# Optimization experiments

Hardware: AMD Instinct MI355X
Metric: run time of the kernel (lower is better)

## Reference

```python
import jax, jax.numpy as jnp
import numpy as np

N, E, B, H, L = 100000, 200000, 2048, 256, 4
EPS_MSG = 1e-7   # GENConv message eps
LN_EPS = 1e-5    # torch LayerNorm default eps
SM_EPS = 1e-16   # PyG softmax denominator eps


def layer_norm(x, g, b):
    mu = x.mean(-1, keepdims=True)
    var = ((x - mu) ** 2).mean(-1, keepdims=True)
    return (x - mu) * jax.lax.rsqrt(var + LN_EPS) * g + b


def gen_conv(x, src, dst, eattr, t, W1, b1, lg, lb, W2, b2):
    # GENConv(aggr='softmax', learn_t, num_layers=2, norm='layer')
    msg = jax.nn.relu(x[src] + eattr) + EPS_MSG                      # [E,H]
    scaled = msg * t
    seg_max = jax.ops.segment_max(scaled, dst, num_segments=N)       # [N,H]
    seg_max = jnp.where(jnp.isfinite(seg_max), seg_max, 0.0)
    ex = jnp.exp(scaled - seg_max[dst])                              # [E,H]
    denom = jax.ops.segment_sum(ex, dst, num_segments=N)             # [N,H]
    alpha = ex / (denom[dst] + SM_EPS)
    out = jax.ops.segment_sum(msg * alpha, dst, num_segments=N)      # [N,H]
    out = out + x                                                    # root residual inside GENConv
    h = jax.nn.relu(layer_norm(out @ W1 + b1, lg, lb))               # MLP: Lin -> LN -> ReLU -> Lin
    return h @ W2 + b2


def setup_inputs() -> dict:
    key = jax.random.key(0)
    ks = iter(jax.random.split(key, 16))
    s = lambda *sh: jax.random.normal(next(ks), sh, jnp.float32) * 0.05
    return dict(
        x=jax.random.normal(next(ks), (N, 9), jnp.float32),
        edge_index=jax.random.randint(next(ks), (2, E), 0, N),
        edge_attr=jax.random.normal(next(ks), (E, 3), jnp.float32),
        batch=jnp.sort(jax.random.randint(next(ks), (N,), 0, B)),
        node_W=s(9, H), node_b=jnp.zeros((H,), jnp.float32),
        edge_W=s(3, H), edge_b=jnp.zeros((H,), jnp.float32),
        vn_emb=jnp.zeros((1, H), jnp.float32),
        ln_g=jnp.ones((L, H), jnp.float32), ln_b=jnp.zeros((L, H), jnp.float32),
        t=jnp.ones((L - 1,), jnp.float32),
        mlp_W1=s(L - 1, H, 2 * H), mlp_b1=jnp.zeros((L - 1, 2 * H), jnp.float32),
        mlp_ln_g=jnp.ones((L - 1, 2 * H), jnp.float32), mlp_ln_b=jnp.zeros((L - 1, 2 * H), jnp.float32),
        mlp_W2=s(L - 1, 2 * H, H), mlp_b2=jnp.zeros((L - 1, H), jnp.float32),
    )


def reference(x, edge_index, edge_attr, batch, node_W, node_b, edge_W, edge_b,
              vn_emb, ln_g, ln_b, t, mlp_W1, mlp_b1, mlp_ln_g, mlp_ln_b, mlp_W2, mlp_b2):
    src, dst = edge_index[0], edge_index[1]
    h = x @ node_W + node_b                                          # node encoder
    ea = edge_attr @ edge_W + edge_b                                 # edge encoder
    vn = jnp.broadcast_to(vn_emb, (B, H))
    counts = jax.ops.segment_sum(jnp.ones((N,), h.dtype), batch, num_segments=B)
    inv_counts = (1.0 / jnp.maximum(counts, 1.0))[:, None]           # [B,1]
    # layers[1:] run conv (block='res+'); layers[0] supplies only the final norm+act
    for l in range(1, L):
        hn = jax.nn.relu(layer_norm(h, ln_g[l], ln_b[l]))            # dropout=0.1 is a no-op in eval
        h = h + gen_conv(hn, src, dst, ea, t[l - 1],
                         mlp_W1[l - 1], mlp_b1[l - 1], mlp_ln_g[l - 1], mlp_ln_b[l - 1],
                         mlp_W2[l - 1], mlp_b2[l - 1])
        vn = vn + jax.ops.segment_sum(h, batch, num_segments=B) * inv_counts  # scatter_mean
        h = h + vn[batch]                                            # broadcast virtual node
    h = jax.nn.relu(layer_norm(h, ln_g[0], ln_b[0]))
    return jax.ops.segment_sum(h, batch, num_segments=B) * inv_counts  # global_mean_pool [B,H]
```

## Files before the change

### kernel.cpp

```cpp
#include <hip/hip_runtime.h>
#include <cstdint>
#include <cstddef>


typedef _Float16 half8_t __attribute__((ext_vector_type(8)));
typedef _Float16 half4_t __attribute__((ext_vector_type(4)));
typedef float    floatx4 __attribute__((ext_vector_type(4)));

#define DEVINL __device__ __forceinline__

DEVINL float wave_sum(float v) {
#pragma unroll
  for (int m = 32; m; m >>= 1) v += __shfl_xor(v, m, 64);
  return v;
}

__global__ __launch_bounds__(256) void k_node_enc(
    const float* __restrict__ x, const float* __restrict__ W,
    const float* __restrict__ bias, _Float16* __restrict__ h, int Nr) {
  __shared__ float sW[9 * 256];
  __shared__ float sb[256];
  __shared__ float sx[72];
  const int j = threadIdx.x;
#pragma unroll
  for (int k = 0; k < 9; ++k) sW[k * 256 + j] = W[k * 256 + j];
  sb[j] = bias[j];
  const int row0 = blockIdx.x * 8;
  if (j < 72) {
    int p = row0 * 9 + j;
    sx[j] = (p < Nr * 9) ? x[p] : 0.f;
  }
  __syncthreads();
  for (int r = 0; r < 8; ++r) {
    int row = row0 + r;
    if (row >= Nr) break;
    float acc = sb[j];
#pragma unroll
    for (int k = 0; k < 9; ++k) acc = fmaf(sx[r * 9 + k], sW[k * 256 + j], acc);
    h[(size_t)row * 256 + j] = (_Float16)acc;
  }
}

__global__ void k_bptr(const int* __restrict__ batch, int* __restrict__ bptr,
                       int N_, int B_) {
  int b = blockIdx.x * 256 + threadIdx.x;
  if (b > B_) return;
  int lo = 0, hi = N_;
  while (lo < hi) {
    int mid = (lo + hi) >> 1;
    if (batch[mid] < b) lo = mid + 1; else hi = mid;
  }
  bptr[b] = lo;
}

__global__ void k_deg(const int* __restrict__ ei, int* __restrict__ deg, int E_) {
  int e = blockIdx.x * 256 + threadIdx.x;
  if (e < E_) atomicAdd(&deg[ei[E_ + e]], 1);
}

__global__ __launch_bounds__(256) void k_scan1(
    const int* __restrict__ in, int* __restrict__ out1, int* __restrict__ bsum, int n) {
  __shared__ int tmp[256];
  const int t = threadIdx.x;
  const int base = blockIdx.x * 1024;
  int v[4];
  int run = 0;
#pragma unroll
  for (int i = 0; i < 4; ++i) {
    int p = base + t * 4 + i;
    int xv = (p < n) ? in[p] : 0;
    run += xv;
    v[i] = run;
  }
  tmp[t] = run;
  __syncthreads();
  for (int off = 1; off < 256; off <<= 1) {
    int u = (t >= off) ? tmp[t - off] : 0;
    __syncthreads();
    tmp[t] += u;
    __syncthreads();
  }
  int excl = tmp[t] - run;
#pragma unroll
  for (int i = 0; i < 4; ++i) {
    int p = base + t * 4 + i;
    if (p < n) out1[p] = v[i] + excl;
  }
  if (t == 255) bsum[blockIdx.x] = tmp[255];
}

__global__ void k_scan2(int* bsum, int nb, int* ptr0) {
  if (threadIdx.x == 0 && blockIdx.x == 0) {
    int run = 0;
    for (int i = 0; i < nb; ++i) { int xv = bsum[i]; bsum[i] = run; run += xv; }
    ptr0[0] = 0;
  }
}

__global__ __launch_bounds__(256) void k_scan3(int* out1, const int* __restrict__ bsum, int n) {
  int add = bsum[blockIdx.x];
  int p0 = blockIdx.x * 1024 + threadIdx.x * 4;
#pragma unroll
  for (int i = 0; i < 4; ++i) {
    int p = p0 + i;
    if (p < n) out1[p] += add;
  }
}

__global__ void k_copy(const int* __restrict__ a, int* __restrict__ b, int n) {
  int i = blockIdx.x * 256 + threadIdx.x;
  if (i < n) b[i] = a[i];
}

__global__ void k_csrfill(const int* __restrict__ ei, int* __restrict__ cursor,
                          int* __restrict__ csr_src, int* __restrict__ csr_eid, int E_) {
  int e = blockIdx.x * 256 + threadIdx.x;
  if (e < E_) {
    int d = ei[E_ + e];
    int pos = atomicAdd(&cursor[d], 1);
    csr_src[pos] = ei[e];
    csr_eid[pos] = e;
  }
}

__global__ void k_vninit(const float* __restrict__ emb, float* __restrict__ vn) {
  vn[(size_t)blockIdx.x * 256 + threadIdx.x] = emb[threadIdx.x];
}

__global__ __launch_bounds__(256) void k_wcvt_all(
    const float* __restrict__ W1, const float* __restrict__ W2,
    _Float16* __restrict__ W1T, _Float16* __restrict__ W2T) {
  int idx = blockIdx.x * 256 + threadIdx.x;
  int mat = idx >> 17;
  int rem = idx & 131071;
  if (mat < 3) {
    int k = rem >> 9, n = rem & 511;
    W1T[(size_t)mat * 131072 + (size_t)n * 256 + k] =
        (_Float16)W1[(size_t)mat * 131072 + rem];
  } else {
    int m = mat - 3;
    int k = rem >> 8, n = rem & 255;
    W2T[(size_t)m * 131072 + (size_t)n * 512 + k] =
        (_Float16)W2[(size_t)m * 131072 + rem];
  }
}

__global__ __launch_bounds__(256) void k_ln256(
    const _Float16* __restrict__ h, const float* __restrict__ g,
    const float* __restrict__ b, _Float16* __restrict__ out, int Nr) {
  int row = blockIdx.x * 4 + (threadIdx.x >> 6);
  if (row >= Nr) return;
  int lane = threadIdx.x & 63;
  half4_t xh = *(const half4_t*)(h + (size_t)row * 256 + lane * 4);
  float x0 = (float)xh[0], x1 = (float)xh[1], x2 = (float)xh[2], x3 = (float)xh[3];
  float s = wave_sum(x0 + x1 + x2 + x3);
  float mu = s * (1.f / 256.f);
  float d0 = x0 - mu, d1 = x1 - mu, d2 = x2 - mu, d3 = x3 - mu;
  float v = wave_sum(d0 * d0 + d1 * d1 + d2 * d2 + d3 * d3);
  float rstd = rsqrtf(v * (1.f / 256.f) + 1e-5f);
  float4 gv = *(const float4*)(g + lane * 4);
  float4 bv = *(const float4*)(b + lane * 4);
  half4_t o;
  o[0] = (_Float16)fmaxf(d0 * rstd * gv.x + bv.x, 0.f);
  o[1] = (_Float16)fmaxf(d1 * rstd * gv.y + bv.y, 0.f);
  o[2] = (_Float16)fmaxf(d2 * rstd * gv.z + bv.z, 0.f);
  o[3] = (_Float16)fmaxf(d3 * rstd * gv.w + bv.w, 0.f);
  *(half4_t*)(out + (size_t)row * 256 + lane * 4) = o;
}

__global__ __launch_bounds__(256) void k_aggregate(
    const _Float16* __restrict__ hn, const float* __restrict__ eattr,
    const float* __restrict__ edgeW, const float* __restrict__ edgeB,
    const int* __restrict__ indptr, const int* __restrict__ csr_src,
    const int* __restrict__ csr_eid, const float* __restrict__ tptr,
    _Float16* __restrict__ agg, int Nr) {
  int node = blockIdx.x * 4 + (threadIdx.x >> 6);
  if (node >= Nr) return;
  int lane = threadIdx.x & 63;
  int j0 = lane * 4;
  float4 w0 = *(const float4*)(edgeW + j0);
  float4 w1 = *(const float4*)(edgeW + 256 + j0);
  float4 w2 = *(const float4*)(edgeW + 512 + j0);
  float4 wb = *(const float4*)(edgeB + j0);
  float W0[4] = {w0.x, w0.y, w0.z, w0.w};
  float W1r[4] = {w1.x, w1.y, w1.z, w1.w};
  float W2r[4] = {w2.x, w2.y, w2.z, w2.w};
  float WB[4] = {wb.x, wb.y, wb.z, wb.w};
  float tval = tptr[0];
  int e0 = indptr[node], e1 = indptr[node + 1];
  float D[4] = {0.f, 0.f, 0.f, 0.f};
  float Nu[4] = {0.f, 0.f, 0.f, 0.f};
  for (int s = e0; s < e1; ++s) {
    int srcn = csr_src[s];
    int eid = csr_eid[s];
    float ex0 = eattr[(size_t)eid * 3 + 0];
    float ex1 = eattr[(size_t)eid * 3 + 1];
    float ex2 = eattr[(size_t)eid * 3 + 2];
    half4_t hv = *(const half4_t*)(hn + (size_t)srcn * 256 + j0);
#pragma unroll
    for (int i = 0; i < 4; ++i) {
      float eaj = fmaf(ex0, W0[i], fmaf(ex1, W1r[i], fmaf(ex2, W2r[i], WB[i])));
      float msg = fmaxf((float)hv[i] + eaj, 0.f) + 1e-7f;
      float pr = __expf(msg * tval);
      D[i] += pr;
      Nu[i] = fmaf(pr, msg, Nu[i]);
    }
  }
  half4_t hs = *(const half4_t*)(hn + (size_t)node * 256 + j0);
  half4_t res;
#pragma unroll
  for (int i = 0; i < 4; ++i)
    res[i] = (_Float16)(Nu[i] / (D[i] + 1e-16f) + (float)hs[i]);
  *(half4_t*)(agg + (size_t)node * 256 + j0) = res;
}

__global__ __launch_bounds__(256, 3) void k_gemm1(
    const _Float16* __restrict__ A, const _Float16* __restrict__ BT,
    const float* __restrict__ bias, _Float16* __restrict__ outh,
    float2* __restrict__ rstat, int M) {
  __shared__ _Float16 ldsA[64 * 256];
  __shared__ _Float16 ldsB[128 * 64];
  const int tid = threadIdx.x;
  const int lane = tid & 63;
  const int wv = tid >> 6;
  const int m0 = blockIdx.x * 64;
  const int wm = wv * 16;
  const int q = lane >> 4;
  const int l16 = lane & 15;

  {
    half8_t tmp[8];
    int ss[8];
#pragma unroll
    for (int g = 0; g < 8; ++g) {
      int s = g * 256 + tid;
      int r = s >> 5;
      int c = (s & 31) ^ (r & 7);
      int rowA = m0 + r;
      rowA = rowA < M ? rowA : (M - 1);
      tmp[g] = *(const half8_t*)(A + (size_t)rowA * 256 + c * 8);
      ss[g] = s;
    }
#pragma unroll
    for (int g = 0; g < 8; ++g)
      *(half8_t*)(ldsA + (size_t)ss[g] * 8) = tmp[g];
  }

  size_t offB[4];
  int ldsOffB[4];
#pragma unroll
  for (int i = 0; i < 4; ++i) {
    int p = (i * 4 + wv) * 64 + lane;
    int r = p >> 3;
    int s = p & 7;
    int gg = s ^ (r & 7);
    offB[i] = (size_t)r * 256 + gg * 8;
    ldsOffB[i] = p * 8;
  }
  half8_t rb[4];
  auto loadB = [&](int j) {
    int n = j >> 2, t = j & 3;
    size_t base = (size_t)n * 128 * 256 + t * 64;
#pragma unroll
    for (int i = 0; i < 4; ++i)
      rb[i] = *(const half8_t*)(BT + base + offB[i]);
  };
  auto writeB = [&]() {
#pragma unroll
    for (int i = 0; i < 4; ++i)
      *(half8_t*)(ldsB + ldsOffB[i]) = rb[i];
  };

  floatx4 acc[8] = {};
  float sA[4] = {0.f, 0.f, 0.f, 0.f}, s2A[4] = {0.f, 0.f, 0.f, 0.f};

  loadB(0);
  writeB();
  for (int j = 0; j < 16; ++j) {
    __syncthreads();
    if (j + 1 < 16) loadB(j + 1);
    const int t = j & 3;
#pragma unroll
    for (int kk = 0; kk < 2; ++kk) {
      const int c8 = kk * 4 + q;
      const int cg = t * 8 + c8;
      int r = wm + l16;
      half8_t af = *(const half8_t*)(ldsA + (size_t)(r * 32 + (cg ^ (r & 7))) * 8);
      half8_t bf[8];
#pragma unroll
      for (int ct = 0; ct < 8; ++ct) {
        int n = ct * 16 + l16;
        bf[ct] = *(const half8_t*)(ldsB + (size_t)(n * 8 + (c8 ^ (n & 7))) * 8);
      }
#pragma unroll
      for (int ct = 0; ct < 8; ++ct)
        acc[ct] = __builtin_amdgcn_mfma_f32_16x16x32_f16(af, bf[ct], acc[ct], 0, 0, 0);
    }
    __syncthreads();
    if (j + 1 < 16) writeB();
    if ((j & 3) == 3) {
      int n = j >> 2;
#pragma unroll
      for (int rr = 0; rr < 4; ++rr) {
        int row = m0 + wm + q * 4 + rr;
        float vv[8];
        float s = 0.f, s2 = 0.f;
#pragma unroll
        for (int ct = 0; ct < 8; ++ct) {
          int col = n * 128 + ct * 16 + l16;
          float v = acc[ct][rr] + bias[col];
          vv[ct] = v;
          s += v;
          s2 += v * v;
        }
        if (row < M) {
#pragma unroll
          for (int ct = 0; ct < 8; ++ct) {
            int col = n * 128 + ct * 16 + l16;
            outh[(size_t)row * 512 + col] = (_Float16)vv[ct];
          }
        }
        sA[rr] += s;
        s2A[rr] += s2;
      }
#pragma unroll
      for (int ct = 0; ct < 8; ++ct)
        acc[ct] = floatx4{0.f, 0.f, 0.f, 0.f};
    }
  }

#pragma unroll
  for (int rr = 0; rr < 4; ++rr) {
    float s = sA[rr], s2 = s2A[rr];
#pragma unroll
    for (int m = 1; m < 16; m <<= 1) {
      s += __shfl_xor(s, m, 64);
      s2 += __shfl_xor(s2, m, 64);
    }
    int row = m0 + wm + q * 4 + rr;
    if (l16 == 0 && row < M) rstat[row] = make_float2(s, s2);
  }
}

template <int VN>
__global__ __launch_bounds__(256, 2) void k_gemm2(
    const _Float16* __restrict__ A, const _Float16* __restrict__ BT,
    const float* __restrict__ bias, const float2* __restrict__ rstat,
    const float* __restrict__ lg, const float* __restrict__ lb,
    const float* __restrict__ vn, const int* __restrict__ batch,
    _Float16* __restrict__ outf, int M) {
  constexpr int K = 512, NN = 256, NT = K / 64;
  constexpr int EPS = 68;
  const int g = blockIdx.x;
  const int mI = blockIdx.y * 8 + (g & 7);
  const int nI = g >> 3;
  const int mT = (M + 127) >> 7;
  if (mI >= mT) return;

  __shared__ _Float16 ldsbuf[4 * 64 * EPS];
  _Float16* ldsA = ldsbuf;
  _Float16* ldsB = ldsbuf + 128 * 64;
  __shared__ float sg[512];
  __shared__ float sbt[512];
  const int tid = threadIdx.x;
  sg[tid] = lg[tid];
  sg[tid + 256] = lg[tid + 256];
  sbt[tid] = lb[tid];
  sbt[tid + 256] = lb[tid + 256];
  __syncthreads();

  const int lane = tid & 63;
  const int wv = tid >> 6;
  const int m0 = mI * 128;
  const int n0 = nI * 128;
  const int wm = (wv >> 1) * 64;
  const int wn = (wv & 1) * 64;
  const int q = lane >> 4;
  const int l16 = lane & 15;
  floatx4 acc[4][4] = {};

  size_t offA[4], offB[4];
  int ldsOff[4], gcolA[4];
  float aco[4], cco[4];
#pragma unroll
  for (int i = 0; i < 4; ++i) {
    int p = (i * 4 + wv) * 64 + lane;
    int r = p >> 3;
    int s = p & 7;
    int gg = s ^ (r & 7);
    int rowA = m0 + r;
    rowA = rowA < M ? rowA : (M - 1);
    offA[i] = (size_t)rowA * K + gg * 8;
    offB[i] = (size_t)(n0 + r) * K + gg * 8;
    ldsOff[i] = p * 8;
    gcolA[i] = gg * 8;
    float2 st = rstat[rowA];
    float mu = st.x * (1.f / 512.f);
    float var = st.y * (1.f / 512.f) - mu * mu;
    float rs = rsqrtf(var + 1e-5f);
    aco[i] = rs;
    cco[i] = -mu * rs;
  }
  half8_t ra[4], rb[4];
  auto loadtile = [&](int kt) {
#pragma unroll
    for (int i = 0; i < 4; ++i) {
      ra[i] = *(const half8_t*)(A + offA[i] + kt);
      rb[i] = *(const half8_t*)(BT + offB[i] + kt);
    }
  };
  auto writetile = [&](int kt) {
#pragma unroll
    for (int i = 0; i < 4; ++i) {
      int c0 = kt + gcolA[i];
      half8_t ya;
#pragma unroll
      for (int jj = 0; jj < 8; ++jj) {
        float e = fmaf((float)ra[i][jj], aco[i], cco[i]);
        float y = fmaf(e, sg[c0 + jj], sbt[c0 + jj]);
        ya[jj] = (_Float16)fmaxf(y, 0.f);
      }
      *(half8_t*)(ldsA + ldsOff[i]) = ya;
      *(half8_t*)(ldsB + ldsOff[i]) = rb[i];
    }
  };

  loadtile(0);
  writetile(0);
#pragma unroll
  for (int t = 0; t < NT; ++t) {
    __syncthreads();
    if (t + 1 < NT) loadtile((t + 1) * 64);
#pragma unroll
    for (int kk = 0; kk < 2; ++kk) {
      half8_t af[4], bf[4];
      const int c8 = kk * 4 + q;
#pragma unroll
      for (int rt = 0; rt < 4; ++rt) {
        int r = wm + rt * 16 + l16;
        af[rt] = *(const half8_t*)(ldsA + (size_t)(r * 8 + (c8 ^ (r & 7))) * 8);
      }
#pragma unroll
      for (int ct = 0; ct < 4; ++ct) {
        int n = wn + ct * 16 + l16;
        bf[ct] = *(const half8_t*)(ldsB + (size_t)(n * 8 + (c8 ^ (n & 7))) * 8);
      }
#pragma unroll
      for (int rt = 0; rt < 4; ++rt)
#pragma unroll
        for (int ct = 0; ct < 4; ++ct)
          acc[rt][ct] = __builtin_amdgcn_mfma_f32_16x16x32_f16(af[rt], bf[ct], acc[rt][ct], 0, 0, 0);
    }
    __syncthreads();
    if (t + 1 < NT) writetile((t + 1) * 64);
  }

  _Float16* epi = ldsbuf + wv * (64 * EPS);
#pragma unroll
  for (int rt = 0; rt < 4; ++rt) {
#pragma unroll
    for (int rr = 0; rr < 4; ++rr) {
      int rloc = rt * 16 + q * 4 + rr;
      int row = m0 + wm + rloc;
      int rowc = row < M ? row : (M - 1);
      int bb = 0;
      if constexpr (VN) bb = batch[rowc];
#pragma unroll
      for (int ct = 0; ct < 4; ++ct) {
        int cloc = ct * 16 + l16;
        int col = n0 + wn + cloc;
        float v = acc[rt][ct][rr] + bias[col];
        if constexpr (VN) v += vn[(size_t)bb * 256 + col];
        epi[rloc * EPS + cloc] = (_Float16)v;
      }
    }
  }
#pragma unroll
  for (int it = 0; it < 8; ++it) {
    int rloc = it * 8 + (lane >> 3);
    int row = m0 + wm + rloc;
    if (row < M) {
      int c0 = (lane & 7) * 8;
      size_t gidx = (size_t)row * NN + n0 + wn + c0;
      half8_t hv = *(const half8_t*)(outf + gidx);
      half8_t ev = *(const half8_t*)(epi + rloc * EPS + c0);
      half8_t o;
#pragma unroll
      for (int jj = 0; jj < 8; ++jj) o[jj] = (_Float16)((float)hv[jj] + (float)ev[jj]);
      *(half8_t*)(outf + gidx) = o;
    }
  }
}

__global__ __launch_bounds__(256) void k_vnln(
    const _Float16* __restrict__ h, float* __restrict__ vn,
    const int* __restrict__ bptr, const float* __restrict__ g,
    const float* __restrict__ b, _Float16* __restrict__ hn) {
  __shared__ float red[3][256];
  __shared__ float svn[256];
  int bb = blockIdx.x;
  int w = threadIdx.x >> 6;
  int lane = threadIdx.x & 63;
  int n0 = bptr[bb], n1 = bptr[bb + 1];
  float a0 = 0.f, a1 = 0.f, a2 = 0.f, a3 = 0.f;
  for (int row = n0 + w; row < n1; row += 4) {
    half4_t xh = *(const half4_t*)(h + (size_t)row * 256 + lane * 4);
    a0 += (float)xh[0]; a1 += (float)xh[1];
    a2 += (float)xh[2]; a3 += (float)xh[3];
  }
  if (w > 0) {
    red[w - 1][lane * 4 + 0] = a0;
    red[w - 1][lane * 4 + 1] = a1;
    red[w - 1][lane * 4 + 2] = a2;
    red[w - 1][lane * 4 + 3] = a3;
  }
  __syncthreads();
  if (w == 0) {
    int c = n1 - n0;
    float ic = 1.f / (float)(c > 1 ? c : 1);
#pragma unroll
    for (int k = 0; k < 3; ++k) {
      a0 += red[k][lane * 4 + 0];
      a1 += red[k][lane * 4 + 1];
      a2 += red[k][lane * 4 + 2];
      a3 += red[k][lane * 4 + 3];
    }
    float4 vo = *(const float4*)(vn + (size_t)bb * 256 + lane * 4);
    vo.x += a0 * ic; vo.y += a1 * ic; vo.z += a2 * ic; vo.w += a3 * ic;
    *(float4*)(vn + (size_t)bb * 256 + lane * 4) = vo;
    svn[lane * 4 + 0] = vo.x;
    svn[lane * 4 + 1] = vo.y;
    svn[lane * 4 + 2] = vo.z;
    svn[lane * 4 + 3] = vo.w;
  }
  __syncthreads();
  float4 vv = *(const float4*)(svn + lane * 4);
  float4 gv = *(const float4*)(g + lane * 4);
  float4 bv = *(const float4*)(b + lane * 4);
  for (int row = n0 + w; row < n1; row += 4) {
    half4_t xh = *(const half4_t*)(h + (size_t)row * 256 + lane * 4);
    float x0 = (float)xh[0] + vv.x, x1 = (float)xh[1] + vv.y;
    float x2 = (float)xh[2] + vv.z, x3 = (float)xh[3] + vv.w;
    float s = wave_sum(x0 + x1 + x2 + x3);
    float mu = s * (1.f / 256.f);
    float d0 = x0 - mu, d1 = x1 - mu, d2 = x2 - mu, d3 = x3 - mu;
    float v = wave_sum(d0 * d0 + d1 * d1 + d2 * d2 + d3 * d3);
    float rstd = rsqrtf(v * (1.f / 256.f) + 1e-5f);
    half4_t o;
    o[0] = (_Float16)fmaxf(d0 * rstd * gv.x + bv.x, 0.f);
    o[1] = (_Float16)fmaxf(d1 * rstd * gv.y + bv.y, 0.f);
    o[2] = (_Float16)fmaxf(d2 * rstd * gv.z + bv.z, 0.f);
    o[3] = (_Float16)fmaxf(d3 * rstd * gv.w + bv.w, 0.f);
    *(half4_t*)(hn + (size_t)row * 256 + lane * 4) = o;
  }
}

__global__ __launch_bounds__(256) void k_vnlnpool(
    const _Float16* __restrict__ h, const float* __restrict__ vn,
    const int* __restrict__ bptr, const float* __restrict__ g,
    const float* __restrict__ b, float* __restrict__ out) {
  __shared__ float red[3][256];
  __shared__ float svn[256];
  int bb = blockIdx.x;
  int w = threadIdx.x >> 6;
  int lane = threadIdx.x & 63;
  int n0 = bptr[bb], n1 = bptr[bb + 1];
  int c = n1 - n0;
  float ic = 1.f / (float)(c > 1 ? c : 1);
  float a0 = 0.f, a1 = 0.f, a2 = 0.f, a3 = 0.f;
  for (int row = n0 + w; row < n1; row += 4) {
    half4_t xh = *(const half4_t*)(h + (size_t)row * 256 + lane * 4);
    a0 += (float)xh[0]; a1 += (float)xh[1];
    a2 += (float)xh[2]; a3 += (float)xh[3];
  }
  if (w > 0) {
    red[w - 1][lane * 4 + 0] = a0;
    red[w - 1][lane * 4 + 1] = a1;
    red[w - 1][lane * 4 + 2] = a2;
    red[w - 1][lane * 4 + 3] = a3;
  }
  __syncthreads();
  if (w == 0) {
#pragma unroll
    for (int k = 0; k < 3; ++k) {
      a0 += red[k][lane * 4 + 0];
      a1 += red[k][lane * 4 + 1];
      a2 += red[k][lane * 4 + 2];
      a3 += red[k][lane * 4 + 3];
    }
    float4 vo = *(const float4*)(vn + (size_t)bb * 256 + lane * 4);
    svn[lane * 4 + 0] = vo.x + a0 * ic;
    svn[lane * 4 + 1] = vo.y + a1 * ic;
    svn[lane * 4 + 2] = vo.z + a2 * ic;
    svn[lane * 4 + 3] = vo.w + a3 * ic;
  }
  __syncthreads();
  float4 vv = *(const float4*)(svn + lane * 4);
  float4 gv = *(const float4*)(g + lane * 4);
  float4 bv = *(const float4*)(b + lane * 4);
  a0 = a1 = a2 = a3 = 0.f;
  for (int row = n0 + w; row < n1; row += 4) {
    half4_t xh = *(const half4_t*)(h + (size_t)row * 256 + lane * 4);
    float x0 = (float)xh[0] + vv.x, x1 = (float)xh[1] + vv.y;
    float x2 = (float)xh[2] + vv.z, x3 = (float)xh[3] + vv.w;
    float s = wave_sum(x0 + x1 + x2 + x3);
    float mu = s * (1.f / 256.f);
    float d0 = x0 - mu, d1 = x1 - mu, d2 = x2 - mu, d3 = x3 - mu;
    float v = wave_sum(d0 * d0 + d1 * d1 + d2 * d2 + d3 * d3);
    float rstd = rsqrtf(v * (1.f / 256.f) + 1e-5f);
    a0 += fmaxf(d0 * rstd * gv.x + bv.x, 0.f);
    a1 += fmaxf(d1 * rstd * gv.y + bv.y, 0.f);
    a2 += fmaxf(d2 * rstd * gv.z + bv.z, 0.f);
    a3 += fmaxf(d3 * rstd * gv.w + bv.w, 0.f);
  }
  __syncthreads();
  if (w > 0) {
    red[w - 1][lane * 4 + 0] = a0;
    red[w - 1][lane * 4 + 1] = a1;
    red[w - 1][lane * 4 + 2] = a2;
    red[w - 1][lane * 4 + 3] = a3;
  }
  __syncthreads();
  if (w == 0) {
#pragma unroll
    for (int k = 0; k < 3; ++k) {
      a0 += red[k][lane * 4 + 0];
      a1 += red[k][lane * 4 + 1];
      a2 += red[k][lane * 4 + 2];
      a3 += red[k][lane * 4 + 3];
    }
    float4 o = {a0 * ic, a1 * ic, a2 * ic, a3 * ic};
    *(float4*)(out + (size_t)bb * 256 + lane * 4) = o;
  }
}

extern "C" void kernel_launch(void* const* d_in, const int* in_sizes, int n_in,
                              void* d_out, int out_size, void* d_ws, size_t ws_size,
                              hipStream_t stream) {
  const float* x      = (const float*)d_in[0];
  const int*   ei     = (const int*)d_in[1];
  const float* eattr  = (const float*)d_in[2];
  const int*   batch  = (const int*)d_in[3];
  const float* nodeW  = (const float*)d_in[4];
  const float* nodeB  = (const float*)d_in[5];
  const float* edgeW  = (const float*)d_in[6];
  const float* edgeB  = (const float*)d_in[7];
  const float* vnemb  = (const float*)d_in[8];
  const float* lng    = (const float*)d_in[9];
  const float* lnb    = (const float*)d_in[10];
  const float* tparam = (const float*)d_in[11];
  const float* W1     = (const float*)d_in[12];
  const float* b1     = (const float*)d_in[13];
  const float* mlng   = (const float*)d_in[14];
  const float* mlnb   = (const float*)d_in[15];
  const float* W2     = (const float*)d_in[16];
  const float* b2     = (const float*)d_in[17];
  float* out = (float*)d_out;

  const int N = in_sizes[3];
  const int E = in_sizes[1] / 2;
  const int B = out_size / 256;

  char* p = (char*)d_ws;
  auto take = [&](size_t bytes) -> char* {
    char* r = p;
    p += (bytes + 255) & ~(size_t)255;
    return r;
  };
  _Float16*  h   = (_Float16*)take((size_t)N * 256 * 2);
  _Float16*  t1  = (_Float16*)take((size_t)N * 512 * 2);
  _Float16*  hn  = t1;
  _Float16*  agg = (_Float16*)take((size_t)N * 256 * 2);
  _Float16*  W1T = (_Float16*)take((size_t)3 * 512 * 256 * 2);
  _Float16*  W2T = (_Float16*)take((size_t)3 * 256 * 512 * 2);
  float2*    rstat = (float2*)take((size_t)N * 8);
  float*     vn  = (float*)take((size_t)B * 256 * 4);
  int*       bptr   = (int*)take((size_t)(B + 1) * 4);
  int*       deg    = (int*)take((size_t)N * 4);
  int*       indptr = (int*)take((size_t)(N + 1) * 4);
  int*       cursor = (int*)take((size_t)N * 4);
  int*       csr_src = (int*)take((size_t)E * 4);
  int*       csr_eid = (int*)take((size_t)E * 4);
  int*       bsum    = (int*)take(512 * 4);
  (void)ws_size; (void)n_in;

  hipMemsetAsync(deg, 0, (size_t)N * 4, stream);

  k_node_enc<<<(N + 7) / 8, 256, 0, stream>>>(x, nodeW, nodeB, h, N);
  k_bptr<<<(B + 256) / 256, 256, 0, stream>>>(batch, bptr, N, B);

  const int nbN = (N + 1023) / 1024;
  k_deg<<<(E + 255) / 256, 256, 0, stream>>>(ei, deg, E);
  k_scan1<<<nbN, 256, 0, stream>>>(deg, indptr + 1, bsum, N);
  k_scan2<<<1, 64, 0, stream>>>(bsum, nbN, indptr);
  k_scan3<<<nbN, 256, 0, stream>>>(indptr + 1, bsum, N);
  k_copy<<<(N + 255) / 256, 256, 0, stream>>>(indptr, cursor, N);
  k_csrfill<<<(E + 255) / 256, 256, 0, stream>>>(ei, cursor, csr_src, csr_eid, E);

  k_wcvt_all<<<3072, 256, 0, stream>>>(W1, W2, W1T, W2T);
  k_vninit<<<B, 256, 0, stream>>>(vnemb, vn);

  const int lnGrid = (N + 3) / 4;
  const int mTiles1 = (N + 63) / 64;
  const int mTiles2 = (N + 127) / 128;
  const dim3 g2grid(16, (mTiles2 + 7) / 8);

  k_ln256<<<lnGrid, 256, 0, stream>>>(h, lng + 256, lnb + 256, hn, N);
  for (int l = 1; l <= 3; ++l) {
    k_aggregate<<<lnGrid, 256, 0, stream>>>(hn, eattr, edgeW, edgeB, indptr, csr_src, csr_eid,
                                            tparam + (l - 1), agg, N);
    k_gemm1<<<mTiles1, 256, 0, stream>>>(
        agg, W1T + (size_t)(l - 1) * 512 * 256, b1 + (size_t)(l - 1) * 512, t1, rstat, N);
    if (l == 1)
      k_gemm2<0><<<g2grid, 256, 0, stream>>>(
          t1, W2T + (size_t)(l - 1) * 256 * 512, b2 + (size_t)(l - 1) * 256, rstat,
          mlng + (size_t)(l - 1) * 512, mlnb + (size_t)(l - 1) * 512, nullptr, nullptr, h, N);
    else
      k_gemm2<1><<<g2grid, 256, 0, stream>>>(
          t1, W2T + (size_t)(l - 1) * 256 * 512, b2 + (size_t)(l - 1) * 256, rstat,
          mlng + (size_t)(l - 1) * 512, mlnb + (size_t)(l - 1) * 512, vn, batch, h, N);
    if (l < 3)
      k_vnln<<<B, 256, 0, stream>>>(h, vn, bptr,
                                    lng + (size_t)(l + 1) * 256, lnb + (size_t)(l + 1) * 256, hn);
    else
      k_vnlnpool<<<B, 256, 0, stream>>>(h, vn, bptr, lng, lnb, out);
  }
}
```

Baseline: 760.3 us.

## Fuse MLP GEMM1, LayerNorm+ReLU and GEMM2 into one kernel keeping intermediate in LDS

After: 848.4 us. 11.6% more time.

```diff
diff --git a/kernel.cpp b/kernel.cpp
--- a/kernel.cpp
+++ b/kernel.cpp
@@ -214,26 +214,42 @@
   *(half4_t*)(agg + (size_t)node * 256 + j0) = res;
 }
 
-__global__ __launch_bounds__(256, 3) void k_gemm1(
-    const _Float16* __restrict__ A, const _Float16* __restrict__ BT,
-    const float* __restrict__ bias, _Float16* __restrict__ outh,
-    float2* __restrict__ rstat, int M) {
-  __shared__ _Float16 ldsA[64 * 256];
-  __shared__ _Float16 ldsB[128 * 64];
+template <int VN>
+__global__ __launch_bounds__(512, 2) void k_fused(
+    const _Float16* __restrict__ A, const _Float16* __restrict__ B1T,
+    const float* __restrict__ b1, const float* __restrict__ lg,
+    const float* __restrict__ lb, const _Float16* __restrict__ B2T,
+    const float* __restrict__ b2, const float* __restrict__ vn,
+    const int* __restrict__ batch, _Float16* __restrict__ outf, int M) {
+  __shared__ _Float16 ldsT1[64 * 512];
+  __shared__ _Float16 ldsS[2048 * 8];
+  __shared__ _Float16 ldsB1[1024 * 8];
+  __shared__ float sb1[512];
+  __shared__ float sg[512];
+  __shared__ float sbt[512];
+  __shared__ float sb2[256];
+  __shared__ float sstat[64 * 4];
+
   const int tid = threadIdx.x;
   const int lane = tid & 63;
   const int wv = tid >> 6;
-  const int m0 = blockIdx.x * 64;
-  const int wm = wv * 16;
   const int q = lane >> 4;
   const int l16 = lane & 15;
+  const int m0 = blockIdx.x * 64;
+  const int wm = (wv >> 1) * 16;
+  const int cg = wv & 1;
+
+  sb1[tid] = b1[tid];
+  sg[tid] = lg[tid];
+  sbt[tid] = lb[tid];
+  if (tid < 256) sb2[tid] = b2[tid];
 
   {
-    half8_t tmp[8];
-    int ss[8];
-#pragma unroll
-    for (int g = 0; g < 8; ++g) {
-      int s = g * 256 + tid;
+    half8_t tmp[4];
+    int ss[4];
+#pragma unroll
+    for (int g = 0; g < 4; ++g) {
+      int s = g * 512 + tid;
       int r = s >> 5;
       int c = (s & 31) ^ (r & 7);
       int rowA = m0 + r;
@@ -242,90 +258,81 @@
       ss[g] = s;
     }
 #pragma unroll
-    for (int g = 0; g < 8; ++g)
-      *(half8_t*)(ldsA + (size_t)ss[g] * 8) = tmp[g];
-  }
-
-  size_t offB[4];
-  int ldsOffB[4];
-#pragma unroll
-  for (int i = 0; i < 4; ++i) {
-    int p = (i * 4 + wv) * 64 + lane;
+    for (int g = 0; g < 4; ++g)
+      *(half8_t*)(ldsS + (size_t)ss[g] * 8) = tmp[g];
+  }
+
+  size_t offB[2];
+  int ldsOffB[2];
+#pragma unroll
+  for (int i = 0; i < 2; ++i) {
+    int p = i * 512 + tid;
     int r = p >> 3;
     int s = p & 7;
     int gg = s ^ (r & 7);
     offB[i] = (size_t)r * 256 + gg * 8;
     ldsOffB[i] = p * 8;
   }
-  half8_t rb[4];
-  auto loadB = [&](int j) {
+  half8_t rb[2];
+  auto loadB1 = [&](int j) {
     int n = j >> 2, t = j & 3;
-    size_t base = (size_t)n * 128 * 256 + t * 64;
-#pragma unroll
-    for (int i = 0; i < 4; ++i)
-      rb[i] = *(const half8_t*)(BT + base + offB[i]);
+    size_t base = (size_t)n * 128 * 256 + (size_t)t * 64;
+#pragma unroll
+    for (int i = 0; i < 2; ++i)
+      rb[i] = *(const half8_t*)(B1T + base + offB[i]);
   };
-  auto writeB = [&]() {
-#pragma unroll
-    for (int i = 0; i < 4; ++i)
-      *(half8_t*)(ldsB + ldsOffB[i]) = rb[i];
+  auto writeB1 = [&]() {
+#pragma unroll
+    for (int i = 0; i < 2; ++i)
+      *(half8_t*)(ldsB1 + ldsOffB[i]) = rb[i];
   };
 
-  floatx4 acc[8] = {};
+  floatx4 acc[4] = {};
   float sA[4] = {0.f, 0.f, 0.f, 0.f}, s2A[4] = {0.f, 0.f, 0.f, 0.f};
-
-  loadB(0);
-  writeB();
+  const int wn1 = cg * 64;
+
+  loadB1(0);
+  writeB1();
   for (int j = 0; j < 16; ++j) {
     __syncthreads();
-    if (j + 1 < 16) loadB(j + 1);
+    if (j + 1 < 16) loadB1(j + 1);
     const int t = j & 3;
 #pragma unroll
     for (int kk = 0; kk < 2; ++kk) {
       const int c8 = kk * 4 + q;
-      const int cg = t * 8 + c8;
+      const int ck = t * 8 + c8;
       int r = wm + l16;
-      half8_t af = *(const half8_t*)(ldsA + (size_t)(r * 32 + (cg ^ (r & 7))) * 8);
-      half8_t bf[8];
-#pragma unroll
-      for (int ct = 0; ct < 8; ++ct) {
-        int n = ct * 16 + l16;
-        bf[ct] = *(const half8_t*)(ldsB + (size_t)(n * 8 + (c8 ^ (n & 7))) * 8);
+      half8_t af = *(const half8_t*)(ldsS + (size_t)(r * 32 + (ck ^ (r & 7))) * 8);
+      half8_t bf[4];
+#pragma unroll
+      for (int ct = 0; ct < 4; ++ct) {
+        int n = wn1 + ct * 16 + l16;
+        bf[ct] = *(const half8_t*)(ldsB1 + (size_t)(n * 8 + (c8 ^ (n & 7))) * 8);
       }
 #pragma unroll
-      for (int ct = 0; ct < 8; ++ct)
+      for (int ct = 0; ct < 4; ++ct)
         acc[ct] = __builtin_amdgcn_mfma_f32_16x16x32_f16(af, bf[ct], acc[ct], 0, 0, 0);
     }
     __syncthreads();
-    if (j + 1 < 16) writeB();
+    if (j + 1 < 16) writeB1();
     if ((j & 3) == 3) {
       int n = j >> 2;
 #pragma unroll
       for (int rr = 0; rr < 4; ++rr) {
-        int row = m0 + wm + q * 4 + rr;
-        float vv[8];
-        float s = 0.f, s2 = 0.f;
-#pragma unroll
-        for (int ct = 0; ct < 8; ++ct) {
-          int col = n * 128 + ct * 16 + l16;
-          float v = acc[ct][rr] + bias[col];
-          vv[ct] = v;
-          s += v;
-          s2 += v * v;
+        int rloc = wm + q * 4 + rr;
+#pragma unroll
+        for (int ct = 0; ct < 4; ++ct) {
+          int col = n * 128 + wn1 + ct * 16 + l16;
+          float v = acc[ct][rr] + sb1[col];
+          sA[rr] += v;
+          s2A[rr] += v * v;
+          int cch = col >> 3;
+          int slot = (cch & 56) | ((cch & 7) ^ (rloc & 7));
+          ldsT1[(size_t)rloc * 512 + slot * 8 + (col & 7)] = (_Float16)v;
         }
-        if (row < M) {
-#pragma unroll
-          for (int ct = 0; ct < 8; ++ct) {
-            int col = n * 128 + ct * 16 + l16;
-            outh[(size_t)row * 512 + col] = (_Float16)vv[ct];
-          }
-        }
-        sA[rr] += s;
-        s2A[rr] += s2;
       }
 #pragma unroll
-      for (int ct = 0; ct < 8; ++ct)
-        acc[ct] = floatx4{0.f, 0.f, 0.f, 0.f};
+      for (int ct = 0; ct < 4; ++ct) acc[ct] = floatx4{0.f, 0.f, 0.f, 0.f};
     }
   }
 
@@ -337,153 +344,115 @@
       s += __shfl_xor(s, m, 64);
       s2 += __shfl_xor(s2, m, 64);
     }
-    int row = m0 + wm + q * 4 + rr;
-    if (l16 == 0 && row < M) rstat[row] = make_float2(s, s2);
-  }
-}
-
-template <int VN>
-__global__ __launch_bounds__(256, 2) void k_gemm2(
-    const _Float16* __restrict__ A, const _Float16* __restrict__ BT,
-    const float* __restrict__ bias, const float2* __restrict__ rstat,
-    const float* __restrict__ lg, const float* __restrict__ lb,
-    const float* __restrict__ vn, const int* __restrict__ batch,
-    _Float16* __restrict__ outf, int M) {
-  constexpr int K = 512, NN = 256, NT = K / 64;
-  constexpr int EPS = 68;
-  const int g = blockIdx.x;
-  const int mI = blockIdx.y * 8 + (g & 7);
-  const int nI = g >> 3;
-  const int mT = (M + 127) >> 7;
-  if (mI >= mT) return;
-
-  __shared__ _Float16 ldsbuf[4 * 64 * EPS];
-  _Float16* ldsA = ldsbuf;
-  _Float16* ldsB = ldsbuf + 128 * 64;
-  __shared__ float sg[512];
-  __shared__ float sbt[512];
-  const int tid = threadIdx.x;
-  sg[tid] = lg[tid];
-  sg[tid + 256] = lg[tid + 256];
-  sbt[tid] = lb[tid];
-  sbt[tid + 256] = lb[tid + 256];
-  __syncthreads();
-
-  const int lane = tid & 63;
-  const int wv = tid >> 6;
-  const int m0 = mI * 128;
-  const int n0 = nI * 128;
-  const int wm = (wv >> 1) * 64;
-  const int wn = (wv & 1) * 64;
-  const int q = lane >> 4;
-  const int l16 = lane & 15;
-  floatx4 acc[4][4] = {};
-
-  size_t offA[4], offB[4];
-  int ldsOff[4], gcolA[4];
-  float aco[4], cco[4];
+    if (l16 == 0) {
+      int rloc = wm + q * 4 + rr;
+      sstat[rloc * 4 + cg * 2 + 0] = s;
+      sstat[rloc * 4 + cg * 2 + 1] = s2;
+    }
+  }
+
+  size_t offB2[4];
+  int ldsOffB2[4];
 #pragma unroll
   for (int i = 0; i < 4; ++i) {
-    int p = (i * 4 + wv) * 64 + lane;
+    int p = i * 512 + tid;
     int r = p >> 3;
     int s = p & 7;
     int gg = s ^ (r & 7);
-    int rowA = m0 + r;
-    rowA = rowA < M ? rowA : (M - 1);
-    offA[i] = (size_t)rowA * K + gg * 8;
-    offB[i] = (size_t)(n0 + r) * K + gg * 8;
-    ldsOff[i] = p * 8;
-    gcolA[i] = gg * 8;
-    float2 st = rstat[rowA];
-    float mu = st.x * (1.f / 512.f);
-    float var = st.y * (1.f / 512.f) - mu * mu;
+    offB2[i] = (size_t)r * 512 + gg * 8;
+    ldsOffB2[i] = p * 8;
+  }
+  half8_t rb2[4];
+  auto loadB2 = [&](int kt) {
+#pragma unroll
+    for (int i = 0; i < 4; ++i)
+      rb2[i] = *(const half8_t*)(B2T + offB2[i] + kt * 64);
+  };
+  auto writeB2 = [&]() {
+#pragma unroll
+    for (int i = 0; i < 4; ++i)
+      *(half8_t*)(ldsS + ldsOffB2[i]) = rb2[i];
+  };
+
+  loadB2(0);
+  __syncthreads();
+  writeB2();
+
+  {
+    int r = tid >> 3;
+    int t7 = tid & 7;
+    float fs = sstat[r * 4 + 0] + sstat[r * 4 + 2];
+    float fs2 = sstat[r * 4 + 1] + sstat[r * 4 + 3];
+    float mu = fs * (1.f / 512.f);
+    float var = fs2 * (1.f / 512.f) - mu * mu;
     float rs = rsqrtf(var + 1e-5f);
-    aco[i] = rs;
-    cco[i] = -mu * rs;
-  }
-  half8_t ra[4], rb[4];
-  auto loadtile = [&](int kt) {
-#pragma unroll
-    for (int i = 0; i < 4; ++i) {
-      ra[i] = *(const half8_t*)(A + offA[i] + kt);
-      rb[i] = *(const half8_t*)(BT + offB[i] + kt);
-    }
-  };
-  auto writetile = [&](int kt) {
-#pragma unroll
-    for (int i = 0; i < 4; ++i) {
-      int c0 = kt + gcolA[i];
-      half8_t ya;
+#pragma unroll
+    for (int g = 0; g < 8; ++g) {
+      int slot = g * 8 + t7;
+      int cch = (slot & 56) | ((slot & 7) ^ (r & 7));
+      half8_t v = *(half8_t*)(ldsT1 + (size_t)r * 512 + slot * 8);
+      half8_t o;
+      int c0 = cch * 8;
 #pragma unroll
       for (int jj = 0; jj < 8; ++jj) {
-        float e = fmaf((float)ra[i][jj], aco[i], cco[i]);
-        float y = fmaf(e, sg[c0 + jj], sbt[c0 + jj]);
-        ya[jj] = (_Float16)fmaxf(y, 0.f);
+        float e = ((float)v[jj] - mu) * rs;
+        o[jj] = (_Float16)fmaxf(fmaf(e, sg[c0 + jj], sbt[c0 + jj]), 0.f);
       }
-      *(half8_t*)(ldsA + ldsOff[i]) = ya;
-      *(half8_t*)(ldsB + ldsOff[i]) = rb[i];
-    }
-  };
-
-  loadtile(0);
-  writetile(0);
-#pragma unroll
-  for (int t = 0; t < NT; ++t) {
+      *(half8_t*)(ldsT1 + (size_t)r * 512 + slot * 8) = o;
+    }
+  }
+
+  floatx4 acc2[8] = {};
+  const int wn2 = cg * 128;
+  for (int kt = 0; kt < 8; ++kt) {
     __syncthreads();
-    if (t + 1 < NT) loadtile((t + 1) * 64);
+    if (kt + 1 < 8) loadB2(kt + 1);
 #pragma unroll
     for (int kk = 0; kk < 2; ++kk) {
-      half8_t af[4], bf[4];
       const int c8 = kk * 4 + q;
-#pragma unroll
-      for (int rt = 0; rt < 4; ++rt) {
-        int r = wm + rt * 16 + l16;
-        af[rt] = *(const half8_t*)(ldsA + (size_t)(r * 8 + (c8 ^ (r & 7))) * 8);
+      int r = wm + l16;
+      half8_t af = *(const half8_t*)(ldsT1 + (size_t)(r * 64 + kt * 8 + (c8 ^ (r & 7))) * 8);
+      half8_t bf[8];
+#pragma unroll
+      for (int ct = 0; ct < 8; ++ct) {
+        int n = wn2 + ct * 16 + l16;
+        bf[ct] = *(const half8_t*)(ldsS + (size_t)(n * 8 + (c8 ^ (n & 7))) * 8);
       }
 #pragma unroll
-      for (int ct = 0; ct < 4; ++ct) {
-        int n = wn + ct * 16 + l16;
-        bf[ct] = *(const half8_t*)(ldsB + (size_t)(n * 8 + (c8 ^ (n & 7))) * 8);
-      }
-#pragma unroll
-      for (int rt = 0; rt < 4; ++rt)
-#pragma unroll
-        for (int ct = 0; ct < 4; ++ct)
-          acc[rt][ct] = __builtin_amdgcn_mfma_f32_16x16x32_f16(af[rt], bf[ct], acc[rt][ct], 0, 0, 0);
+      for (int ct = 0; ct < 8; ++ct)
+        acc2[ct] = __builtin_amdgcn_mfma_f32_16x16x32_f16(af, bf[ct], acc2[ct], 0, 0, 0);
     }
     __syncthreads();
-    if (t + 1 < NT) writetile((t + 1) * 64);
-  }
-
-  _Float16* epi = ldsbuf + wv * (64 * EPS);
-#pragma unroll
-  for (int rt = 0; rt < 4; ++rt) {
-#pragma unroll
-    for (int rr = 0; rr < 4; ++rr) {
-      int rloc = rt * 16 + q * 4 + rr;
-      int row = m0 + wm + rloc;
-      int rowc = row < M ? row : (M - 1);
-      int bb = 0;
-      if constexpr (VN) bb = batch[rowc];
-#pragma unroll
-      for (int ct = 0; ct < 4; ++ct) {
-        int cloc = ct * 16 + l16;
-        int col = n0 + wn + cloc;
-        float v = acc[rt][ct][rr] + bias[col];
-        if constexpr (VN) v += vn[(size_t)bb * 256 + col];
-        epi[rloc * EPS + cloc] = (_Float16)v;
-      }
-    }
-  }
-#pragma unroll
-  for (int it = 0; it < 8; ++it) {
-    int rloc = it * 8 + (lane >> 3);
+    if (kt + 1 < 8) writeB2();
+  }
+
+  constexpr int EPS2 = 136;
+  _Float16* epi = ldsT1 + (size_t)wv * (16 * EPS2);
+#pragma unroll
+  for (int rr = 0; rr < 4; ++rr) {
+    int rloc = q * 4 + rr;
+    int row = m0 + wm + rloc;
+    int rowc = row < M ? row : (M - 1);
+    int bb = 0;
+    if constexpr (VN) bb = batch[rowc];
+#pragma unroll
+    for (int ct = 0; ct < 8; ++ct) {
+      int cloc = ct * 16 + l16;
+      int col = wn2 + cloc;
+      float v = acc2[ct][rr] + sb2[col];
+      if constexpr (VN) v += vn[(size_t)bb * 256 + col];
+      epi[rloc * EPS2 + cloc] = (_Float16)v;
+    }
+  }
+#pragma unroll
+  for (int it = 0; it < 4; ++it) {
+    int rloc = it * 4 + (lane >> 4);
     int row = m0 + wm + rloc;
     if (row < M) {
-      int c0 = (lane & 7) * 8;
-      size_t gidx = (size_t)row * NN + n0 + wn + c0;
+      int c0 = (lane & 15) * 8;
+      size_t gidx = (size_t)row * 256 + wn2 + c0;
       half8_t hv = *(const half8_t*)(outf + gidx);
-      half8_t ev = *(const half8_t*)(epi + rloc * EPS + c0);
+      half8_t ev = *(const half8_t*)(epi + rloc * EPS2 + c0);
       half8_t o;
 #pragma unroll
       for (int jj = 0; jj < 8; ++jj) o[jj] = (_Float16)((float)hv[jj] + (float)ev[jj]);
@@ -668,12 +637,10 @@
     return r;
   };
   _Float16*  h   = (_Float16*)take((size_t)N * 256 * 2);
-  _Float16*  t1  = (_Float16*)take((size_t)N * 512 * 2);
-  _Float16*  hn  = t1;
+  _Float16*  hn  = (_Float16*)take((size_t)N * 256 * 2);
   _Float16*  agg = (_Float16*)take((size_t)N * 256 * 2);
   _Float16*  W1T = (_Float16*)take((size_t)3 * 512 * 256 * 2);
   _Float16*  W2T = (_Float16*)take((size_t)3 * 256 * 512 * 2);
-  float2*    rstat = (float2*)take((size_t)N * 8);
   float*     vn  = (float*)take((size_t)B * 256 * 4);
   int*       bptr   = (int*)take((size_t)(B + 1) * 4);
   int*       deg    = (int*)take((size_t)N * 4);
@@ -701,24 +668,24 @@
   k_vninit<<<B, 256, 0, stream>>>(vnemb, vn);
 
   const int lnGrid = (N + 3) / 4;
-  const int mTiles1 = (N + 63) / 64;
-  const int mTiles2 = (N + 127) / 128;
-  const dim3 g2grid(16, (mTiles2 + 7) / 8);
+  const int mTiles = (N + 63) / 64;
 
   k_ln256<<<lnGrid, 256, 0, stream>>>(h, lng + 256, lnb + 256, hn, N);
   for (int l = 1; l <= 3; ++l) {
     k_aggregate<<<lnGrid, 256, 0, stream>>>(hn, eattr, edgeW, edgeB, indptr, csr_src, csr_eid,
                                             tparam + (l - 1), agg, N);
-    k_gemm1<<<mTiles1, 256, 0, stream>>>(
-        agg, W1T + (size_t)(l - 1) * 512 * 256, b1 + (size_t)(l - 1) * 512, t1, rstat, N);
     if (l == 1)
-      k_gemm2<0><<<g2grid, 256, 0, stream>>>(
-          t1, W2T + (size_t)(l - 1) * 256 * 512, b2 + (size_t)(l - 1) * 256, rstat,
-          mlng + (size_t)(l - 1) * 512, mlnb + (size_t)(l - 1) * 512, nullptr, nullptr, h, N);
+      k_fused<0><<<mTiles, 512, 0, stream>>>(
+          agg, W1T + (size_t)(l - 1) * 512 * 256, b1 + (size_t)(l - 1) * 512,
+          mlng + (size_t)(l - 1) * 512, mlnb + (size_t)(l - 1) * 512,
+          W2T + (size_t)(l - 1) * 256 * 512, b2 + (size_t)(l - 1) * 256,
+          nullptr, nullptr, h, N);
     else
-      k_gemm2<1><<<g2grid, 256, 0, stream>>>(
-          t1, W2T + (size_t)(l - 1) * 256 * 512, b2 + (size_t)(l - 1) * 256, rstat,
-          mlng + (size_t)(l - 1) * 512, mlnb + (size_t)(l - 1) * 512, vn, batch, h, N);
+      k_fused<1><<<mTiles, 512, 0, stream>>>(
+          agg, W1T + (size_t)(l - 1) * 512 * 256, b1 + (size_t)(l - 1) * 512,
+          mlng + (size_t)(l - 1) * 512, mlnb + (size_t)(l - 1) * 512,
+          W2T + (size_t)(l - 1) * 256 * 512, b2 + (size_t)(l - 1) * 256,
+          vn, batch, h, N);
     if (l < 3)
       k_vnln<<<B, 256, 0, stream>>>(h, vn, bptr,
                                     lng + (size_t)(l + 1) * 256, lnb + (size_t)(l + 1) * 256, hn);
```
